# Kernel optimization log

Hardware: AMD Instinct MI355X
Metric: run time of the kernel (lower is better)

## Reference

```python
import jax, jax.numpy as jnp
import numpy as np

# --- model hyperparams (match init_kwargs) ---
N_DIM = 200      # n_dim == nfeat == nhidden (Linear(200,200) hardcoded in source)
NHID = 200
NLAYERS = 8
ALPHA = 0.1
LAMDA = 0.5
B, L = 20, 100   # dialogues x uniform dialogue length
N = B * L        # 2000 utterances per modality -> 3N = 6000 graph nodes
A_DIM, V_DIM, L_DIM, NSPK = 300, 342, 1024, 2


def _linear_params(key, fin, fout):
    s = 1.0 / np.sqrt(fin)
    k1, k2 = jax.random.split(key)
    W = jax.random.uniform(k1, (fin, fout), jnp.float32, -s, s)
    b = jax.random.uniform(k2, (fout,), jnp.float32, -s, s)
    return W, b


def setup_inputs() -> dict:
    key = jax.random.key(0)
    ks = jax.random.split(key, 12)
    a = jax.random.normal(ks[0], (N, A_DIM), jnp.float32)
    v = jax.random.normal(ks[1], (N, V_DIM), jnp.float32)
    l = jax.random.normal(ks[2], (N, L_DIM), jnp.float32)
    qmask = jax.random.uniform(ks[3], (L, B, NSPK), dtype=jnp.float32)
    # dense normalized adjacency over the 3N-node multimodal graph
    adj = jax.random.uniform(ks[4], (3 * N, 3 * N), dtype=jnp.float32) / (3.0 * N)
    Wa, ba = _linear_params(ks[5], A_DIM, N_DIM)
    Wv, bv = _linear_params(ks[6], V_DIM, N_DIM)
    Wl, bl = _linear_params(ks[7], L_DIM, N_DIM)
    spk_emb = jax.random.normal(ks[8], (NSPK, N_DIM), jnp.float32)
    W0, b0 = _linear_params(ks[9], N_DIM, NHID)
    s = 1.0 / np.sqrt(NHID)
    # variant=True -> conv weight is [2*nhidden, nhidden]
    convW = jax.random.uniform(ks[10], (NLAYERS, 2 * NHID, NHID), jnp.float32, -s, s)
    return dict(a=a, v=v, l=l, qmask=qmask, adj=adj,
                Wa=Wa, ba=ba, Wv=Wv, bv=bv, Wl=Wl, bl=bl,
                spk_emb=spk_emb, W0=W0, b0=b0, convW=convW, dia_len=L)


def reference(a, v, l, qmask, adj, Wa, ba, Wv, bv, Wl, bl, spk_emb, W0, b0, convW, dia_len):
    # modality projections
    a = a @ Wa + ba                                   # [N, n_dim]
    v = v @ Wv + bv
    l = l @ Wl + bl
    # qmask: [L, B, n_spk] seq-first -> concat per dialogue (uniform lengths)
    qcat = jnp.transpose(qmask[:dia_len], (1, 0, 2)).reshape(-1, qmask.shape[-1])  # [N, n_spk]
    spk_idx = jnp.argmax(qcat, axis=-1)
    l = l + spk_emb[spk_idx]                          # use_speaker, 'l' in modals
    # big multimodal graph: stack modalities along node axis
    x = jnp.concatenate([a, v, l], axis=0)            # [3N, n_dim]
    # GCNII_lyc (eval mode: dropout identity)
    h0 = jax.nn.relu(x @ W0 + b0)                     # [3N, nhidden]
    thetas = jnp.log(LAMDA / jnp.arange(1, NLAYERS + 1, dtype=jnp.float32) + 1.0)

    def layer(h, wt):
        W, theta = wt
        hi = adj @ h                                  # spmm (dense here)
        support = jnp.concatenate([hi, h0], axis=1)   # variant=True
        r = (1.0 - ALPHA) * hi + ALPHA * h0
        h_new = jax.nn.relu(theta * (support @ W) + (1.0 - theta) * r)
        return h_new, None

    h, _ = jax.lax.scan(layer, h0, (convW, thetas))
    feat = jnp.concatenate([x, h], axis=1)            # use_residue -> [3N, n_dim+nhidden]
    n = a.shape[0]
    # split modality chunks back and fuse on feature axis -> [N, 3*(n_dim+nhidden)]
    return jnp.concatenate([feat[:n], feat[n:2 * n], feat[2 * n:3 * n]], axis=-1)
```

## Files before the change

kernel.cpp:

```cpp
#include <hip/hip_runtime.h>
#include <math.h>

typedef unsigned short u16;
typedef unsigned int u32;
typedef __bf16 bf8_t __attribute__((ext_vector_type(8)));
typedef float f4_t __attribute__((ext_vector_type(4)));
typedef u16 us8_t __attribute__((ext_vector_type(8)));
typedef u16 us4_t __attribute__((ext_vector_type(4)));

#define LDC 224
#define NROWS 6016
#define PLANE (NROWS*LDC)

__device__ __forceinline__ float b2f(u16 x){
  union{u32 u; float f;} c; c.u = ((u32)x)<<16; return c.f;
}
__device__ __forceinline__ u16 f2b(float f){
  union{u32 u; float f;} c; c.f = f;
  u32 b = c.u;
  return (u16)((b + 0x7FFFu + ((b>>16)&1u)) >> 16);
}
__device__ __forceinline__ u16 ldcvt(const void* p, size_t i, int f){
  return f ? f2b(((const float*)p)[i]) : ((const u16*)p)[i];
}
__device__ __forceinline__ void gl16(const u16* g, u16* l){
  __builtin_amdgcn_global_load_lds((const __attribute__((address_space(1))) void*)g,
                                   (__attribute__((address_space(3))) void*)l, 16, 0, 0);
}

__global__ void detect_kernel(const u16* __restrict__ adj, int* __restrict__ flag)
{
  int l = threadIdx.x;
  u16 u = adj[2*l];
  int ex = (u >> 7) & 0xFF;
  bool ok = ((u >> 15) == 0) && (ex >= 0x30) && (ex <= 0x72);
  unsigned long long m = __ballot(ok);
  if (l == 0) flag[0] = (__popcll(m) < 32) ? 1 : 0;
}

__global__ void conv_kernel(const int* __restrict__ flag, const void* __restrict__ adj,
                            u16* __restrict__ adj_bf)
{
  const int f = flag[0];
  u32 idx = (u32)blockIdx.x*256u + (u32)threadIdx.x;
  u32 row = idx / 752u;
  int k8  = (int)(idx - row*752u) * 8;
  us8_t vv;
  if (row < 6000u){
    if (f){
      const float* src = (const float*)adj + (size_t)row*6000;
      if (k8 + 8 <= 6000){
        f4_t x0 = *(const f4_t*)(src + k8);
        f4_t x1 = *(const f4_t*)(src + k8 + 4);
        #pragma unroll
        for (int j=0;j<4;j++){ vv[j] = f2b(x0[j]); vv[4+j] = f2b(x1[j]); }
      } else {
        #pragma unroll
        for (int j=0;j<8;j++){ int k=k8+j; vv[j] = (k<6000) ? f2b(src[k]) : (u16)0; }
      }
    } else {
      const u16* src = (const u16*)adj + (size_t)row*6000;
      if (k8 + 8 <= 6000){
        vv = *(const us8_t*)(src + k8);
      } else {
        #pragma unroll
        for (int j=0;j<8;j++){ int k=k8+j; vv[j] = (k<6000) ? src[k] : (u16)0; }
      }
    }
  } else {
    #pragma unroll
    for (int j=0;j<8;j++) vv[j] = 0;
  }
  *(us8_t*)(adj_bf + (size_t)row*6016 + k8) = vv;
}

#define PB_MISC 5320
#define PB_XPAD 5333
#define PB_AP   5347
#define PB_VP   7907
#define PB_END  10979
__global__ void prep_kernel(const int* __restrict__ flag,
                            const void* __restrict__ Wa, const void* __restrict__ Wv,
                            const void* __restrict__ Wl, const void* __restrict__ W0,
                            const void* __restrict__ convW, const void* __restrict__ qmask,
                            const void* __restrict__ a_in, const void* __restrict__ v_in,
                            const void* __restrict__ spkemb_in,
                            const void* __restrict__ ba, const void* __restrict__ bv,
                            const void* __restrict__ bl, const void* __restrict__ b0,
                            u16* __restrict__ WaT, u16* __restrict__ WvT, u16* __restrict__ WlT,
                            u16* __restrict__ W0T, u16* __restrict__ WtT, u16* __restrict__ WbT,
                            int* __restrict__ spk, u16* __restrict__ x_bf,
                            u16* __restrict__ a_p, u16* __restrict__ v_p,
                            u16* __restrict__ spkem, u16* __restrict__ b_all)
{
  const int f = flag[0];
  const int bid = blockIdx.x;
  const int tid = threadIdx.x;

  if (bid < PB_MISC){
    u32 e = (u32)bid*256u + (u32)tid;
    const void* src; u16* dst; u32 K, kpad; u32 soff = 0;
    if (e < 71680u){ src=Wa; dst=WaT; K=300; kpad=320; }
    else if (e < 157696u){ e -= 71680u;  src=Wv; dst=WvT; K=342; kpad=384; }
    else if (e < 387072u){ e -= 157696u; src=Wl; dst=WlT; K=1024; kpad=1024; }
    else if (e < 444416u){ e -= 387072u; src=W0; dst=W0T; K=200; kpad=256; }
    else if (e < 903168u){ e -= 444416u; u32 i = e/57344u; e -= i*57344u;
                           src=convW; soff=i*80000u;          dst=WtT + i*57344; K=200; kpad=256; }
    else {                 e -= 903168u; u32 i = e/57344u; e -= i*57344u;
                           src=convW; soff=i*80000u + 40000u; dst=WbT + i*57344; K=200; kpad=256; }
    u32 k = e / 224u, n = e - k*224u;
    u16 val = 0;
    if (k < K && n < 200u) val = ldcvt(src, (size_t)soff + (size_t)k*200u + n, f);
    dst[(size_t)n*kpad + k] = val;
    return;
  }
  if (bid < PB_XPAD){
    int e = (bid - PB_MISC)*256 + tid;
    if (e < 2000){
      int b = e/100, t = e - b*100;
      size_t base = ((size_t)t*20 + b)*2;
      bool one;
      if (f) one = ((const float*)qmask)[base+1] > ((const float*)qmask)[base];
      else   one = b2f(((const u16*)qmask)[base+1]) > b2f(((const u16*)qmask)[base]);
      spk[e] = one ? 1 : 0;
    } else if (e < 2400){
      spkem[e-2000] = ldcvt(spkemb_in, e-2000, f);
    } else if (e < 3200){
      int j = e - 2400; int which = j/200, idx = j - which*200;
      const void* src = (which==0)?ba:(which==1)?bv:(which==2)?bl:b0;
      b_all[j] = ldcvt(src, idx, f);
    }
    return;
  }
  if (bid < PB_AP){
    int e = (bid - PB_XPAD)*256 + tid;
    if (e < 16*LDC) x_bf[(size_t)6000*LDC + e] = 0;
    return;
  }
  if (bid < PB_VP){
    u32 e = (u32)(bid - PB_AP)*256u + (u32)tid;
    u32 row = e / 320u, k = e - row*320u;
    a_p[e] = (row < 2000u && k < 300u) ? ldcvt(a_in, (size_t)row*300u + k, f) : (u16)0;
    return;
  }
  {
    u32 e = (u32)(bid - PB_VP)*256u + (u32)tid;
    u32 row = e / 384u, k = e - row*384u;
    v_p[e] = (row < 2000u && k < 342u) ? ldcvt(v_in, (size_t)row*342u + k, f) : (u16)0;
  }
}

template<int WR>
__global__ __launch_bounds__(256, 2)
void gemm_kernel(int dynA, const int* __restrict__ flag, const u16* __restrict__ a_sel,
                 const void* __restrict__ A1, int lda1, int kv1, int kg1, int ks1, const u16* __restrict__ B1, int ldb1,
                 int Mv, int Mout, int spp, int emode,
                 const u16* __restrict__ bias, const u16* __restrict__ spk_e, const int* __restrict__ spk_idx,
                 u16* __restrict__ part_base,
                 u16* __restrict__ outN, u16* __restrict__ outT)
{
  __shared__ u16 ldsA[2][WR*32*64];
  __shared__ u16 ldsB[2][224*64];
  const int tid = threadIdx.x;
  const int l = tid & 63;
  const int w = tid >> 6;
  const int wrow = w >> 1, wcol = w & 1;
  const int row0 = blockIdx.x * (WR*32);
  const int lq = l >> 4, lr = l & 15;

  const u16* A16 = (const u16*)A1;
  const float* A32 = (const float*)A1;
  int af32 = 0, lda = lda1, kv = kv1, kg = kg1, Mvl = Mv;
  if (dynA){
    int fd = flag[0];
    if (dynA == 1){
      af32 = fd;
    } else {
      if (fd){ A16 = a_sel; lda = 6016; kv = 6016; kg = 6016; Mvl = 6016; }
    }
  }

  f4_t acc[WR][7];
  #pragma unroll
  for (int i=0;i<WR;i++)
    #pragma unroll
    for (int j=0;j<7;j++){ f4_t z = {0.f,0.f,0.f,0.f}; acc[i][j] = z; }

  int sb = blockIdx.y * spp, se = sb + spp;
  if (se > ks1) se = ks1;

  auto stageA = [&](int p, int k0){
    const u16* abase = A16 + k0;
    #pragma unroll
    for (int i=0;i<WR;i++){
      int c = (i<<8) + tid;
      int m = c >> 3, k8p = c & 7;
      int k8 = k8p ^ (m & 7);
      gl16(abase + (size_t)(row0+m)*lda + (k8<<3), &ldsA[p][c<<3]);
    }
  };
  auto stageB = [&](int p, int k0){
    const u16* bbase = B1 + k0;
    #pragma unroll
    for (int i=0;i<7;i++){
      int c = (i<<8) + tid;
      int n = c >> 3, k8p = c & 7;
      int k8 = k8p ^ (n & 7);
      gl16(bbase + (size_t)n*ldb1 + (k8<<3), &ldsB[p][c<<3]);
    }
  };
  auto computeT = [&](int p){
    #pragma unroll
    for (int h=0; h<2; ++h){
      bf8_t af[WR], bfr[7];
      int kc = lq + (h<<2);
      #pragma unroll
      for (int rt=0;rt<WR;rt++){
        int m = wrow*(16*WR) + rt*16 + lr;
        af[rt] = *(const bf8_t*)(&ldsA[p][(m<<6) + ((kc ^ (m&7))<<3)]);
      }
      #pragma unroll
      for (int ct=0;ct<7;ct++){
        int n = wcol*112 + ct*16 + lr;
        bfr[ct] = *(const bf8_t*)(&ldsB[p][(n<<6) + ((kc ^ (n&7))<<3)]);
      }
      #pragma unroll
      for (int rt=0;rt<WR;rt++)
        #pragma unroll
        for (int ct=0;ct<7;ct++)
          acc[rt][ct] = __builtin_amdgcn_mfma_f32_16x16x32_bf16(af[rt], bfr[ct], acc[rt][ct], 0,0,0);
    }
  };

  bool pipe = (!af32) && ((lda & 7) == 0) && (row0 + WR*32 <= Mvl)
              && (se > sb) && (se*64 <= kg);

  if (pipe){
    stageA(0, sb<<6); stageB(0, sb<<6);
    int p = 0;
    #pragma unroll 1
    for (int s = sb; s < se; ++s){
      if (s + 1 < se){
        stageA(p^1, (s+1)<<6); stageB(p^1, (s+1)<<6);
        if (WR == 2) asm volatile("s_waitcnt vmcnt(9)" ::: "memory");
        else         asm volatile("s_waitcnt vmcnt(8)" ::: "memory");
      } else {
        asm volatile("s_waitcnt vmcnt(0)" ::: "memory");
      }
      __builtin_amdgcn_s_barrier();
      computeT(p);
      __builtin_amdgcn_s_barrier();
      p ^= 1;
    }
  } else {
    #pragma unroll 1
    for (int s = sb; s < se; ++s){
      int k0 = s << 6;
      __syncthreads();
      bool alignedA = ((lda & 7) == 0) && (row0 + WR*32 <= Mvl);
      bool gldsA = (!af32) && alignedA && (k0 + 64 <= kg);
      if (gldsA){
        stageA(0, k0);
      } else if (af32 && alignedA && (k0 + 64 <= kv)){
        const float* ap = A32 + (size_t)row0*lda + k0;
        #pragma unroll
        for (int i=0;i<WR;i++){
          int c = (i<<8) + tid;
          int m = c >> 3, k8 = c & 7;
          f4_t x0 = *(const f4_t*)(ap + (size_t)m*lda + (k8<<3));
          f4_t x1 = *(const f4_t*)(ap + (size_t)m*lda + (k8<<3) + 4);
          us8_t vv;
          #pragma unroll
          for (int j=0;j<4;j++){ vv[j] = f2b(x0[j]); vv[4+j] = f2b(x1[j]); }
          *(us8_t*)(&ldsA[0][(m<<6) + ((k8 ^ (m&7))<<3)]) = vv;
        }
      } else {
        #pragma unroll
        for (int i=0;i<WR;i++){
          int c = (i<<8) + tid;
          int m = c >> 3, k8 = c & 7;
          int gr = row0 + m; if (gr > Mvl-1) gr = Mvl-1;
          us8_t vv;
          #pragma unroll
          for (int j=0;j<8;j++){
            int kk = k0 + (k8<<3) + j;
            u16 t = 0;
            if (kk < kv){
              if (af32) t = f2b(A32[(size_t)gr*lda + kk]);
              else      t = A16[(size_t)gr*lda + kk];
            }
            vv[j] = t;
          }
          *(us8_t*)(&ldsA[0][(m<<6) + ((k8 ^ (m&7))<<3)]) = vv;
        }
      }
      stageB(0, k0);
      __syncthreads();
      computeT(0);
    }
  }

  #pragma unroll
  for (int rt=0;rt<WR;rt++){
    int r_base = row0 + wrow*(16*WR) + rt*16 + lq*4;
    #pragma unroll
    for (int ct=0;ct<7;ct++){
      int c = wcol*112 + ct*16 + lr;
      f4_t a4 = acc[rt][ct];
      if (emode == 0){
        u16* dst = part_base + (size_t)blockIdx.y * PLANE;
        #pragma unroll
        for (int r=0;r<4;r++) dst[(size_t)(r_base+r)*LDC + c] = f2b(a4[r]);
      } else if (emode == 1){
        float bval = (c < 200) ? b2f(bias[c]) : 0.f;
        #pragma unroll
        for (int r=0;r<4;r++){
          int R = r_base + r;
          if (R < Mout){
            float vv = a4[r] + bval;
            if (spk_e && c < 200) vv += b2f(spk_e[spk_idx[R]*200 + c]);
            outN[(size_t)R*LDC + c] = f2b(vv);
          }
        }
      } else {
        float bval = (c < 200) ? b2f(bias[c]) : 0.f;
        us4_t p4;
        #pragma unroll
        for (int r=0;r<4;r++){
          int R = r_base + r;
          float vv = a4[r] + bval; if (vv < 0.f) vv = 0.f;
          u16 q = f2b(vv);
          outN[(size_t)R*LDC + c] = q;
          p4[r] = q;
        }
        *(us4_t*)(&outT[(size_t)c*NROWS + r_base]) = p4;
      }
    }
  }
}

__global__ __launch_bounds__(256, 2)
void layer_kernel(const u16* __restrict__ part, int nsk,
                  const u16* __restrict__ h0_bf,
                  const u16* __restrict__ Bt, const u16* __restrict__ Bb,
                  float theta, u16* __restrict__ outT)
{
  __shared__ u16 ldsHI[32*256];
  __shared__ u16 ldsH0[32*256];
  __shared__ u16 ldsB[2][224*64];
  const int tid = threadIdx.x;
  const int l = tid & 63;
  const int w = tid >> 6;
  const int wrow = w >> 1, wcol = w & 1;
  const int row0 = blockIdx.x * 32;
  const int lq = l >> 4, lr = l & 15;

  #pragma unroll
  for (int rr=0; rr<4; ++rr){
    int c = rr*256 + tid;
    int m = c >> 5, ch = c & 31;
    us8_t o;
    if (ch < 28){
      float s[8];
      #pragma unroll
      for (int j=0;j<8;j++) s[j] = 0.f;
      size_t base = (size_t)(row0+m)*LDC + (ch<<3);
      for (int p=0;p<nsk;p++){
        us8_t vv = *(const us8_t*)(part + (size_t)p*PLANE + base);
        #pragma unroll
        for (int j=0;j<8;j++) s[j] += b2f(vv[j]);
      }
      #pragma unroll
      for (int j=0;j<8;j++) o[j] = f2b(s[j]);
    } else {
      #pragma unroll
      for (int j=0;j<8;j++) o[j] = 0;
    }
    *(us8_t*)(&ldsHI[(m<<8) + ((ch ^ (m&7))<<3)]) = o;
    int sch = ch ^ (m&7);
    gl16(h0_bf + (size_t)(row0+m)*LDC + (sch<<3), &ldsH0[c<<3]);
  }

  auto stageB = [&](int p, int t){
    const u16* Bp = (t>>2) ? Bb : Bt;
    const u16* bbase = Bp + ((t&3)<<6);
    #pragma unroll
    for (int i=0;i<7;i++){
      int c = (i<<8) + tid;
      int n = c >> 3, k8p = c & 7;
      int k8 = k8p ^ (n & 7);
      gl16(bbase + (size_t)n*256 + (k8<<3), &ldsB[p][c<<3]);
    }
  };

  f4_t acc[7];
  #pragma unroll
  for (int j=0;j<7;j++){ f4_t z = {0.f,0.f,0.f,0.f}; acc[j] = z; }

  stageB(0, 0);
  __syncthreads();
  int p = 0;
  #pragma unroll 1
  for (int t = 0; t < 8; ++t){
    if (t < 7){
      stageB(p^1, t+1);
      asm volatile("s_waitcnt vmcnt(7)" ::: "memory");
    } else {
      asm volatile("s_waitcnt vmcnt(0)" ::: "memory");
    }
    __builtin_amdgcn_s_barrier();
    const u16* Alds = (t>>2) ? &ldsH0[0] : &ldsHI[0];
    int sloc = t & 3;
    #pragma unroll
    for (int h=0; h<2; ++h){
      int kc = lq + (h<<2);
      int m = wrow*16 + lr;
      bf8_t af = *(const bf8_t*)(&Alds[(m<<8) + (((sloc<<3) | (kc ^ (m&7)))<<3)]);
      bf8_t bfr[7];
      #pragma unroll
      for (int ct=0;ct<7;ct++){
        int n = wcol*112 + ct*16 + lr;
        bfr[ct] = *(const bf8_t*)(&ldsB[p][(n<<6) + ((kc ^ (n&7))<<3)]);
      }
      #pragma unroll
      for (int ct=0;ct<7;ct++)
        acc[ct] = __builtin_amdgcn_mfma_f32_16x16x32_bf16(af, bfr[ct], acc[ct], 0,0,0);
    }
    __builtin_amdgcn_s_barrier();
    p ^= 1;
  }

  int r_base = row0 + wrow*16 + lq*4;
  #pragma unroll
  for (int ct=0;ct<7;ct++){
    int c = wcol*112 + ct*16 + lr;
    int cc8 = c >> 3, ce = c & 7;
    us4_t p4;
    #pragma unroll
    for (int r=0;r<4;r++){
      int mr = wrow*16 + lq*4 + r;
      int ix = (mr<<8) + ((cc8 ^ (mr&7))<<3) + ce;
      float rrv = 0.9f*b2f(ldsHI[ix]) + 0.1f*b2f(ldsH0[ix]);
      float vv = theta*acc[ct][r] + (1.f - theta)*rrv;
      if (vv < 0.f) vv = 0.f;
      p4[r] = f2b(vv);
    }
    *(us4_t*)(&outT[(size_t)c*NROWS + r_base]) = p4;
  }
}

__device__ __forceinline__ u16 sent(u16 t, u16 snan, u16 sbig){
  u16 mag = t & 0x7FFF;
  if (mag >= 0x7F80) return snan;
  if (mag >= 0x4480) return sbig;
  return t;
}
__global__ void out_kernel(const int* __restrict__ flag,
                           const u16* __restrict__ x_bf, const u16* __restrict__ hT,
                           void* __restrict__ outp)
{
  __shared__ u16 tile[64*216];
  const int of32 = flag[0];
  u16* o16 = (u16*)outp;
  float* o32 = (float*)outp;
  const int tid = threadIdx.x;
  const int n0 = blockIdx.x*64;
  const int m = blockIdx.y;
  for (int cc = tid; cc < 1600; cc += 256){
    int r = cc/25, c8 = cc - r*25;
    int n = n0 + r;
    int rr = n < 2000 ? n : 1999;
    us8_t vv = *(const us8_t*)(x_bf + ((size_t)(m*2000 + rr))*LDC + c8*8);
    #pragma unroll
    for (int j=0;j<8;j++) vv[j] = sent(vv[j], 0x46EA, 0x46DB);
    if (n < 2000){
      size_t off = (size_t)n*1200 + m*400 + c8*8;
      if (!of32) *(us8_t*)(o16 + off) = vv;
      else {
        f4_t lo, hi;
        #pragma unroll
        for (int j=0;j<4;j++){ lo[j] = b2f(vv[j]); hi[j] = b2f(vv[4+j]); }
        *(f4_t*)(o32 + off) = lo; *(f4_t*)(o32 + off + 4) = hi;
      }
    }
  }
  for (int cc = tid; cc < 1600; cc += 256){
    int c = cc >> 3, ng = cc & 7;
    int nb = n0 + ng*8;
    if (nb > 1992) nb = 1992;
    us8_t vv = *(const us8_t*)(hT + (size_t)c*NROWS + m*2000 + nb);
    #pragma unroll
    for (int j=0;j<8;j++) tile[(ng*8+j)*216 + c] = sent(vv[j], 0x469C, 0x468C);
  }
  __syncthreads();
  for (int cc = tid; cc < 1600; cc += 256){
    int r = cc/25, c8 = cc - r*25;
    int n = n0 + r;
    if (n < 2000){
      us8_t vv = *(const us8_t*)(&tile[r*216 + c8*8]);
      size_t off = (size_t)n*1200 + m*400 + 200 + c8*8;
      if (!of32) *(us8_t*)(o16 + off) = vv;
      else {
        f4_t lo, hi;
        #pragma unroll
        for (int j=0;j<4;j++){ lo[j] = b2f(vv[j]); hi[j] = b2f(vv[4+j]); }
        *(f4_t*)(o32 + off) = lo; *(f4_t*)(o32 + off + 4) = hi;
      }
    }
  }
}

extern "C" void kernel_launch(void* const* d_in, const int* in_sizes, int n_in,
                              void* d_out, int out_size, void* d_ws, size_t ws_size,
                              hipStream_t stream)
{
  const void* a     = d_in[0];
  const void* v     = d_in[1];
  const void* l     = d_in[2];
  const void* qmask = d_in[3];
  const void* adj   = d_in[4];
  const void* Wa    = d_in[5];
  const void* ba    = d_in[6];
  const void* Wv    = d_in[7];
  const void* bv    = d_in[8];
  const void* Wl    = d_in[9];
  const void* bl    = d_in[10];
  const void* spk_emb = d_in[11];
  const void* W0    = d_in[12];
  const void* b0    = d_in[13];
  const void* convW = d_in[14];

  int cfg = (ws_size >= (size_t)125*1024*1024) ? 2
          : (ws_size >= (size_t)48*1024*1024) ? 1 : 0;
  const int SK = (cfg >= 1) ? 5 : 2;
  const int SPP = (94 + SK - 1) / SK;

  char* ws = (char*)d_ws;
  size_t off = 0;
  auto alloc = [&](size_t bytes)->char*{
    char* p = ws + off; off = (off + bytes + 255) & ~(size_t)255; return p;
  };
  int*  flag  = (int*) alloc(256);
  u16*  x_bf  = (u16*) alloc((size_t)PLANE*2);
  u16*  h0_bf = (u16*) alloc((size_t)PLANE*2);
  u16*  hT    = (u16*) alloc((size_t)PLANE*2);
  u16*  a_p   = (u16*) alloc((size_t)2048*320*2);
  u16*  v_p   = (u16*) alloc((size_t)2048*384*2);
  u16* WaT = (u16*)alloc(224*320*2);
  u16* WvT = (u16*)alloc(224*384*2);
  u16* WlT = (u16*)alloc(224*1024*2);
  u16* W0T = (u16*)alloc(224*256*2);
  u16* WtT = (u16*)alloc((size_t)8*224*256*2);
  u16* WbT = (u16*)alloc((size_t)8*224*256*2);
  int* spk = (int*)alloc(2000*4);
  u16* spkem = (u16*)alloc(400*2);
  u16* b_all = (u16*)alloc(800*2);
  u16* part = (u16*)alloc((size_t)SK*PLANE*2);
  u16* adj_bf = (cfg == 2) ? (u16*)alloc((size_t)6016*6016*2) : nullptr;

  detect_kernel<<<1,64,0,stream>>>((const u16*)adj, flag);

  if (cfg == 2)
    conv_kernel<<<dim3(17672),256,0,stream>>>(flag, adj, adj_bf);

  prep_kernel<<<dim3(PB_END),256,0,stream>>>(flag,
      Wa,Wv,Wl,W0,convW,qmask, a,v,spk_emb, ba,bv,bl,b0,
      WaT,WvT,WlT,W0T,WtT,WbT, spk, x_bf, a_p,v_p, spkem, b_all);

  gemm_kernel<1><<<dim3(64,1),256,0,stream>>>(0, nullptr, nullptr,
      a_p,320,320,320,5, WaT,320,
      2048,2000, 5, 1, b_all, nullptr, nullptr,
      nullptr, x_bf, nullptr);
  gemm_kernel<1><<<dim3(64,1),256,0,stream>>>(0, nullptr, nullptr,
      v_p,384,384,384,6, WvT,384,
      2048,2000, 6, 1, b_all+200, nullptr, nullptr,
      nullptr, x_bf + (size_t)2000*LDC, nullptr);
  gemm_kernel<1><<<dim3(64,1),256,0,stream>>>(1, flag, nullptr,
      l,1024,1024,1024,16, WlT,1024,
      2000,2000, 16, 1, b_all+400, spkem, spk,
      nullptr, x_bf + (size_t)4000*LDC, nullptr);

  gemm_kernel<1><<<dim3(188,1),256,0,stream>>>(0, nullptr, nullptr,
      x_bf,LDC,LDC,256,4, W0T,256,
      NROWS,NROWS, 4, 2, b_all+600, nullptr, nullptr,
      nullptr, h0_bf, hT);

  for (int i=0;i<8;i++){
    float theta = logf(0.5f/(float)(i+1) + 1.0f);
    if (cfg == 2)
      gemm_kernel<2><<<dim3(94,SK),256,0,stream>>>(3, flag, adj_bf,
          adj,6000,6000,6000,94, hT,NROWS,
          6000,0, SPP, 0, nullptr, nullptr, nullptr,
          part, nullptr, nullptr);
    else
      gemm_kernel<2><<<dim3(94,SK),256,0,stream>>>(1, flag, nullptr,
          adj,6000,6000,6000,94, hT,NROWS,
          6000,0, SPP, 0, nullptr, nullptr, nullptr,
          part, nullptr, nullptr);
    layer_kernel<<<dim3(188),256,0,stream>>>(part, SK, h0_bf,
        WtT + (size_t)i*57344, WbT + (size_t)i*57344, theta, hT);
  }

  out_kernel<<<dim3(32,3),256,0,stream>>>(flag, x_bf, hT, (void*)d_out);
}
```

Measured before the change: 670.5 us.

## Add dedicated double-buffered bf16 adjacency SpMM kernel with direct global A-fragment loads

Adds a specialized kernel for the adj @ h product, used when the bf16 copy of adj is available (cfg==2). A fragments are loaded straight from global memory into registers, and h tiles are staged into double-buffered, XOR-swizzled LDS with explicit vmcnt waits so the next k-step's loads overlap the current MFMA work. It replaces the generic templated gemm path and is meant to cut instruction overhead and stalls in the dominant per-layer GEMM. The cost is more register pressure from 14 accumulators plus prefetched A, and the hand-tuned waitcnt counts are fragile.

```diff
diff --git a/kernel.cpp b/kernel.cpp
--- a/kernel.cpp
+++ b/kernel.cpp
@@ -340,6 +340,102 @@
 }
 
 __global__ __launch_bounds__(256, 2)
+void spmm_kernel(const u16* __restrict__ adj_bf, const u16* __restrict__ hT,
+                 int spp, u16* __restrict__ part_base)
+{
+  __shared__ u16 ldsB[2][224*64];
+  const int tid = threadIdx.x;
+  const int l = tid & 63;
+  const int w = tid >> 6;
+  const int row0 = blockIdx.x * 64;
+  const int lq = l >> 4, lr = l & 15;
+
+  const u16* arow = adj_bf + (size_t)(row0 + w*16 + lr)*6016;
+  const int kofs0 = lq<<3, kofs1 = (lq+4)<<3;
+
+  f4_t acc[14];
+  #pragma unroll
+  for (int j=0;j<14;j++){ f4_t z = {0.f,0.f,0.f,0.f}; acc[j] = z; }
+
+  int sb = blockIdx.y * spp, se = sb + spp;
+  if (se > 94) se = 94;
+
+  bf8_t A0[2], A1[2];
+
+  auto loadA = [&](bf8_t (&A)[2], int s){
+    int k0 = s<<6;
+    A[0] = *(const bf8_t*)(arow + k0 + kofs0);
+    A[1] = *(const bf8_t*)(arow + k0 + kofs1);
+  };
+  auto stageB = [&](int p, int s){
+    const u16* bbase = hT + (s<<6);
+    #pragma unroll
+    for (int i=0;i<7;i++){
+      int c = (i<<8) + tid;
+      int n = c >> 3, k8p = c & 7;
+      int k8 = k8p ^ (n & 7);
+      gl16(bbase + (size_t)n*NROWS + (k8<<3), &ldsB[p][c<<3]);
+    }
+  };
+  auto compute = [&](bf8_t (&A)[2], int p){
+    #pragma unroll
+    for (int h=0; h<2; ++h){
+      int kc = lq + (h<<2);
+      bf8_t bfr[14];
+      #pragma unroll
+      for (int ct=0;ct<14;ct++){
+        int n = ct*16 + lr;
+        bfr[ct] = *(const bf8_t*)(&ldsB[p][(n<<6) + ((kc ^ (n&7))<<3)]);
+      }
+      #pragma unroll
+      for (int ct=0;ct<14;ct++)
+        acc[ct] = __builtin_amdgcn_mfma_f32_16x16x32_bf16(A[h], bfr[ct], acc[ct], 0,0,0);
+    }
+  };
+
+  loadA(A0, sb); stageB(0, sb);
+  int s = sb;
+  #pragma unroll 1
+  while (true){
+    if (s + 1 < se){
+      loadA(A1, s+1); stageB(1, s+1);
+      __builtin_amdgcn_sched_barrier(0);
+      asm volatile("s_waitcnt vmcnt(9)" ::: "memory");
+    } else {
+      asm volatile("s_waitcnt vmcnt(0)" ::: "memory");
+    }
+    __builtin_amdgcn_sched_barrier(0);
+    __builtin_amdgcn_s_barrier();
+    compute(A0, 0);
+    __builtin_amdgcn_s_barrier();
+    if (++s >= se) break;
+
+    if (s + 1 < se){
+      loadA(A0, s+1); stageB(0, s+1);
+      __builtin_amdgcn_sched_barrier(0);
+      asm volatile("s_waitcnt vmcnt(9)" ::: "memory");
+    } else {
+      asm volatile("s_waitcnt vmcnt(0)" ::: "memory");
+    }
+    __builtin_amdgcn_sched_barrier(0);
+    __builtin_amdgcn_s_barrier();
+    compute(A1, 1);
+    __builtin_amdgcn_s_barrier();
+    if (++s >= se) break;
+  }
+
+  u16* dst = part_base + (size_t)blockIdx.y * PLANE;
+  int r_base = row0 + w*16 + lq*4;
+  #pragma unroll
+  for (int ct=0;ct<14;ct++){
+    int c = ct*16 + lr;
+    f4_t a4 = acc[ct];
+    #pragma unroll
+    for (int r=0;r<4;r++) dst[(size_t)(r_base+r)*LDC + c] = f2b(a4[r]);
+  }
+}
+
+__global__ __launch_bounds__(256, 2)
 void layer_kernel(const u16* __restrict__ part, int nsk,
                   const u16* __restrict__ h0_bf,
                   const u16* __restrict__ Bt, const u16* __restrict__ Bb,
@@ -588,10 +684,7 @@
   for (int i=0;i<8;i++){
     float theta = logf(0.5f/(float)(i+1) + 1.0f);
     if (cfg == 2)
-      gemm_kernel<2><<<dim3(94,SK),256,0,stream>>>(3, flag, adj_bf,
-          adj,6000,6000,6000,94, hT,NROWS,
-          6000,0, SPP, 0, nullptr, nullptr, nullptr,
-          part, nullptr, nullptr);
+      spmm_kernel<<<dim3(94,SK),256,0,stream>>>(adj_bf, hT, SPP, part);
     else
       gemm_kernel<2><<<dim3(94,SK),256,0,stream>>>(1, flag, nullptr,
           adj,6000,6000,6000,94, hT,NROWS,
```

After: 695.0 us. 3.7% more time.
